# Kernel tuning notes

Measured on AMD Instinct MI355X. Metric: run time of the kernel, lower is better.

The kernel has to match this reference:

```python
import jax, jax.numpy as jnp
import numpy as np

B, L, H, DK, DV, DM = 8, 1024, 8, 80, 80, 640
LN_EPS = 1e-5


def setup_inputs() -> dict:
    key = jax.random.key(0)
    ks = jax.random.split(key, 5)
    q = jax.random.normal(ks[0], (B, L, DM), dtype=jnp.float32)
    k = jax.random.normal(ks[1], (B, L, DM), dtype=jnp.float32)
    v = jax.random.normal(ks[2], (B, L, DM), dtype=jnp.float32)
    # fc: nn.Linear(n_head*d_v, d_model), xavier-normal init
    fc_std = float(np.sqrt(2.0 / (H * DV + DM)))
    fc_w = jax.random.normal(ks[3], (DM, H * DV), dtype=jnp.float32) * fc_std
    fc_b = jnp.zeros((DM,), dtype=jnp.float32)
    gamma_1 = jnp.full((DM,), 1e-4, dtype=jnp.float32)  # init_values * ones(640)
    ln_w = jnp.ones((DM,), dtype=jnp.float32)
    ln_b = jnp.zeros((DM,), dtype=jnp.float32)
    return {"q": q, "k": k, "v": v, "fc_w": fc_w, "fc_b": fc_b,
            "gamma_1": gamma_1, "ln_w": ln_w, "ln_b": ln_b}


def reference(q, k, v, fc_w, fc_b, gamma_1, ln_w, ln_b):
    # Inputs are viewed directly into heads (projections are commented out in source).
    residual = q
    qh = q.reshape(B, L, H, DK)  # [b, q, h, d]
    kh = k.reshape(B, L, H, DK)  # [b, k, h, d]
    vh = v.reshape(B, L, H, DV)  # [b, k, h, d]

    # L2-distance attention scores: -sum((q-k)^2) = -(||q||^2 - 2 q.k + ||k||^2)
    sq = jnp.sum(qh * qh, axis=-1)                       # [b, q, h]
    sk = jnp.sum(kh * kh, axis=-1)                       # [b, k, h]
    cross = jnp.einsum('bqhd,bkhd->bhqk', qh, kh)        # [b, h, q, k]
    scores = -(sq.transpose(0, 2, 1)[:, :, :, None]
               - 2.0 * cross
               + sk.transpose(0, 2, 1)[:, :, None, :]) / 13.0

    attn = jax.nn.softmax(scores, axis=-1)               # softmax over keys (dim=2 in 3D view)
    # dropout(p=0.8) treated as identity (eval mode)

    out = jnp.einsum('bhqk,bkhd->bqhd', attn, vh)        # [b, q, h, dv]
    out = out.reshape(B, L, H * DV)
    out = out @ fc_w.T + fc_b                            # fc projection
    # dropout treated as identity (eval mode)

    x = out * gamma_1 + residual
    mu = jnp.mean(x, axis=-1, keepdims=True)
    var = jnp.mean((x - mu) ** 2, axis=-1, keepdims=True)
    y = (x - mu) * jax.lax.rsqrt(var + LN_EPS) * ln_w + ln_b
    return y
```

## Files before the change

kernel.cpp:

```cpp
#include <hip/hip_runtime.h>

#define B_ 8
#define L_ 1024
#define H_ 8
#define DM_ 640

typedef __attribute__((ext_vector_type(8))) short bf16x8;
typedef __attribute__((ext_vector_type(4))) short bf16x4;
typedef __attribute__((ext_vector_type(4))) float f32x4;
typedef __attribute__((ext_vector_type(2))) float f32x2;
typedef __attribute__((ext_vector_type(2))) int i32x2;
typedef __attribute__((ext_vector_type(4))) unsigned short us4;
typedef __attribute__((ext_vector_type(8))) unsigned short us8;

#if __has_builtin(__builtin_amdgcn_exp2f)
#define EXP2F __builtin_amdgcn_exp2f
#else
#define EXP2F exp2f
#endif

#define C1F 0.22195308f
#define C2F 0.11097654f

#define VTP_TILE_SHORTS 5184
#define ATTN8_OFF 10616832

__device__ __forceinline__ unsigned short f2bf(float f) {
  unsigned int u = __builtin_bit_cast(unsigned int, f);
  u += 0x7fffu + ((u >> 16) & 1u);
  return (unsigned short)(u >> 16);
}
__device__ __forceinline__ float bf2f(unsigned short h) {
  unsigned int u = ((unsigned int)h) << 16;
  return __builtin_bit_cast(float, u);
}
__device__ __forceinline__ float sane(float x, float lim) {
  return fminf(fmaxf(x, -lim), lim);
}
__device__ __forceinline__ unsigned cvt_pk_bf16(float a, float b) {
  unsigned r;
  asm("v_cvt_pk_bf16_f32 %0, %1, %2" : "=v"(r) : "v"(a), "v"(b));
  return r;
}

__global__ __launch_bounds__(256) void prep_kernel(
    const float* __restrict__ kg, const float* __restrict__ vg,
    unsigned short* __restrict__ Kp, unsigned short* __restrict__ Vtp) {
  __shared__ float V_lds[64 * 81];
  __shared__ float w_lds[64];
  const int tid = threadIdx.x;
  const int bh = blockIdx.x >> 4, kt = blockIdx.x & 15;
  const int b = bh >> 3, h = bh & 7;
  const int key = tid >> 2, part = tid & 3;
  const int keyg = kt * 64 + key;

  const float* krow = kg + (size_t)(b * L_ + keyg) * DM_ + h * 80 + part * 20;
  const float* vrow = vg + (size_t)(b * L_ + keyg) * DM_ + h * 80 + part * 20;
  unsigned short* kpr = Kp + ((size_t)bh * L_ + keyg) * 80 + part * 20;

  float ssq = 0.f;
#pragma unroll
  for (int i = 0; i < 5; ++i) {
    float4 f = *(const float4*)(krow + 4 * i);
    ssq += f.x * f.x + f.y * f.y + f.z * f.z + f.w * f.w;
    us4 h4 = {f2bf(f.x * C1F), f2bf(f.y * C1F), f2bf(f.z * C1F), f2bf(f.w * C1F)};
    *(us4*)(kpr + 4 * i) = h4;
    float4 g4 = *(const float4*)(vrow + 4 * i);
    int d0 = part * 20 + 4 * i;
    V_lds[key * 81 + d0 + 0] = g4.x;
    V_lds[key * 81 + d0 + 1] = g4.y;
    V_lds[key * 81 + d0 + 2] = g4.z;
    V_lds[key * 81 + d0 + 3] = g4.w;
  }
  ssq += __shfl_xor(ssq, 1);
  ssq += __shfl_xor(ssq, 2);
  if (part == 0) w_lds[key] = EXP2F((80.f - ssq) * C2F);
  __syncthreads();

  unsigned short* vt = Vtp + (size_t)(bh * 16 + kt) * VTP_TILE_SHORTS;
#pragma unroll
  for (int r = 0; r < 11; ++r) {
    int p = r * 256 + tid;
    if (p < 81 * 32) {
      int dv = p >> 5, kp = (p & 31) * 2;
      float wa = w_lds[kp], wb = w_lds[kp + 1];
      float va = (dv < 80) ? V_lds[kp * 81 + dv] * wa : wa;
      float vb = (dv < 80) ? V_lds[(kp + 1) * 81 + dv] * wb : wb;
      *(unsigned*)(vt + dv * 64 + kp) =
          (unsigned)f2bf(va) | ((unsigned)f2bf(vb) << 16);
    }
  }
}

#define KSTR 104
#define VSTR 76

__global__ __launch_bounds__(256, 2) void attn_kernel(
    const float* __restrict__ qg, const unsigned short* __restrict__ Kp,
    const unsigned short* __restrict__ Vtp, unsigned char* __restrict__ attn8) {
  __shared__ __align__(16) unsigned short K_lds[2][64 * KSTR];
  __shared__ __align__(16) unsigned short Vt_lds[2][80 * VSTR];
  __shared__ __align__(16) unsigned short w_sh[2][64];

  const int tid = threadIdx.x;
  const int wid = tid >> 6, lane = tid & 63;
  const int col = lane & 15, g = lane >> 4;
  const int bx = blockIdx.x;
  const int bh = bx & 63, qt = bx >> 6;
  const int b = bh >> 3, h = bh & 7;

  if (tid < 128) {
    us8 z = {0, 0, 0, 0, 0, 0, 0, 0};
    int bufz = tid >> 6, r = tid & 63;
    *(us8*)&K_lds[bufz][r * KSTR + 80] = z;
    *(us8*)&K_lds[bufz][r * KSTR + 88] = z;
  }

  const int ka0 = tid, ka1 = tid + 256, ka2 = tid + 512;
  const int kr0 = ka0 / 10, kc0 = ka0 - kr0 * 10;
  const int kr1 = ka1 / 10, kc1 = ka1 - kr1 * 10;
  const int kr2 = ka2 / 10, kc2 = ka2 - kr2 * 10;
  const int vr0 = ka0 >> 3, vc0 = ka0 & 7;
  const int vr1 = ka1 >> 3, vc1 = ka1 & 7;
  const int vr2 = ka2 >> 3, vc2 = ka2 & 7;

  const unsigned short* kslice = Kp + (size_t)bh * L_ * 80;
  const unsigned short* vslice = Vtp + (size_t)(bh * 16) * VTP_TILE_SHORTS;

  us8 sk0, sk1, sk2, sv0, sv1, sv2, sw;
  auto load_tile = [&](int kt) {
    const unsigned short* kb = kslice + (size_t)kt * 5120;
    const unsigned short* vb = vslice + (size_t)kt * VTP_TILE_SHORTS;
    sk0 = *(const us8*)(kb + kr0 * 80 + kc0 * 8);
    sk1 = *(const us8*)(kb + kr1 * 80 + kc1 * 8);
    if (tid < 128) sk2 = *(const us8*)(kb + kr2 * 80 + kc2 * 8);
    sv0 = *(const us8*)(vb + vr0 * 64 + vc0 * 8);
    sv1 = *(const us8*)(vb + vr1 * 64 + vc1 * 8);
    if (tid < 128) sv2 = *(const us8*)(vb + vr2 * 64 + vc2 * 8);
    if (tid < 8) sw = *(const us8*)(vb + 5120 + tid * 8);
  };
  auto write_tile = [&](int bf) {
    *(us8*)&K_lds[bf][kr0 * KSTR + kc0 * 8] = sk0;
    *(us8*)&K_lds[bf][kr1 * KSTR + kc1 * 8] = sk1;
    if (tid < 128) *(us8*)&K_lds[bf][kr2 * KSTR + kc2 * 8] = sk2;
    *(us8*)&Vt_lds[bf][vr0 * VSTR + vc0 * 8] = sv0;
    *(us8*)&Vt_lds[bf][vr1 * VSTR + vc1 * 8] = sv1;
    if (tid < 128) *(us8*)&Vt_lds[bf][vr2 * VSTR + vc2 * 8] = sv2;
    if (tid < 8) *(us8*)&w_sh[bf][tid * 8] = sw;
  };

  bf16x8 qa0[3], qa1[3];
  {
    const int qr0 = qt * 128 + wid * 16 + col;
#pragma unroll
    for (int s = 0; s < 2; ++s) {
      const float* qr = qg + (size_t)(b * L_ + qr0 + s * 64) * DM_ + h * 80;
      bf16x8* qa = s ? qa1 : qa0;
#pragma unroll
      for (int c = 0; c < 3; ++c) {
        int d0 = c * 32 + g * 8;
        if (d0 < 80) {
          float4 f0 = *(const float4*)(qr + d0);
          float4 f1 = *(const float4*)(qr + d0 + 4);
          qa[c][0] = (short)f2bf(f0.x); qa[c][1] = (short)f2bf(f0.y);
          qa[c][2] = (short)f2bf(f0.z); qa[c][3] = (short)f2bf(f0.w);
          qa[c][4] = (short)f2bf(f1.x); qa[c][5] = (short)f2bf(f1.y);
          qa[c][6] = (short)f2bf(f1.z); qa[c][7] = (short)f2bf(f1.w);
        } else {
#pragma unroll
          for (int e = 0; e < 8; ++e) qa[c][e] = 0;
        }
      }
    }
  }

  f32x4 acc_o0[5], acc_o1[5];
#pragma unroll
  for (int u = 0; u < 5; ++u) {
    f32x4 z = {0.f, 0.f, 0.f, 0.f};
    acc_o0[u] = z;
    acc_o1[u] = z;
  }
  float lp0 = 0.f, lp1 = 0.f;

  load_tile(0);
  write_tile(0);
  __syncthreads();

  for (int kt = 0; kt < 16; ++kt) {
    const int cur = kt & 1;
    if (kt < 15) load_tile(kt + 1);

    f32x4 accS0[4], accS1[4];
#pragma unroll
    for (int t = 0; t < 4; ++t) {
      f32x4 z = {0.f, 0.f, 0.f, 0.f};
      accS0[t] = z;
      accS1[t] = z;
    }
    __builtin_amdgcn_s_setprio(1);
#pragma unroll
    for (int t = 0; t < 4; ++t)
#pragma unroll
      for (int c = 0; c < 3; ++c) {
        bf16x8 kf = *(const bf16x8*)&K_lds[cur][(t * 16 + col) * KSTR + c * 32 + g * 8];
        accS0[t] = __builtin_amdgcn_mfma_f32_16x16x32_bf16(kf, qa0[c], accS0[t], 0, 0, 0);
        accS1[t] = __builtin_amdgcn_mfma_f32_16x16x32_bf16(kf, qa1[c], accS1[t], 0, 0, 0);
      }
    __builtin_amdgcn_s_setprio(0);

#pragma unroll
    for (int t = 0; t < 4; ++t) {
      us4 w4 = *(const us4*)&w_sh[cur][t * 16 + g * 4];
      float w0 = bf2f(w4[0]), w1 = bf2f(w4[1]), w2 = bf2f(w4[2]), w3 = bf2f(w4[3]);
      float p00 = EXP2F(accS0[t][0]), p01 = EXP2F(accS0[t][1]);
      float p02 = EXP2F(accS0[t][2]), p03 = EXP2F(accS0[t][3]);
      float p10 = EXP2F(accS1[t][0]), p11 = EXP2F(accS1[t][1]);
      float p12 = EXP2F(accS1[t][2]), p13 = EXP2F(accS1[t][3]);
      lp0 += p00 * w0 + p01 * w1 + p02 * w2 + p03 * w3;
      lp1 += p10 * w0 + p11 * w1 + p12 * w2 + p13 * w3;
      i32x2 pw0 = {(int)cvt_pk_bf16(p00, p01), (int)cvt_pk_bf16(p02, p03)};
      i32x2 pw1 = {(int)cvt_pk_bf16(p10, p11), (int)cvt_pk_bf16(p12, p13)};
      bf16x4 pf0 = __builtin_bit_cast(bf16x4, pw0);
      bf16x4 pf1 = __builtin_bit_cast(bf16x4, pw1);
      __builtin_amdgcn_s_setprio(1);
#pragma unroll
      for (int u = 0; u < 5; ++u) {
        bf16x4 vf = *(const bf16x4*)&Vt_lds[cur][(u * 16 + col) * VSTR + t * 16 + g * 4];
        acc_o0[u] = __builtin_amdgcn_mfma_f32_16x16x16bf16_1k(vf, pf0, acc_o0[u], 0, 0, 0);
        acc_o1[u] = __builtin_amdgcn_mfma_f32_16x16x16bf16_1k(vf, pf1, acc_o1[u], 0, 0, 0);
      }
      __builtin_amdgcn_s_setprio(0);
    }

    if (kt < 15) {
      write_tile(cur ^ 1);
      __syncthreads();
    }
  }

  float l0 = lp0 + __shfl_xor(lp0, 16);
  l0 += __shfl_xor(l0, 32);
  float l1 = lp1 + __shfl_xor(lp1, 16);
  l1 += __shfl_xor(l1, 32);
#pragma unroll
  for (int s = 0; s < 2; ++s) {
    f32x4* acc_o = s ? acc_o1 : acc_o0;
    float invl = 1.0f / fmaxf(s ? l1 : l0, 1e-30f);
    const int qrow = qt * 128 + s * 64 + wid * 16 + col;
    unsigned char* ob = attn8 + (size_t)(b * L_ + qrow) * DM_ + h * 80;
#pragma unroll
    for (int u = 0; u < 5; ++u) {
      float o0 = sane(acc_o[u][0] * invl, 240.f);
      float o1 = sane(acc_o[u][1] * invl, 240.f);
      float o2 = sane(acc_o[u][2] * invl, 240.f);
      float o3 = sane(acc_o[u][3] * invl, 240.f);
      int pk = __builtin_amdgcn_cvt_pk_fp8_f32(o0, o1, 0, false);
      pk = __builtin_amdgcn_cvt_pk_fp8_f32(o2, o3, pk, true);
      *(int*)(ob + u * 16 + g * 4) = pk;
    }
  }
}

#define BSTR 40
__global__ __launch_bounds__(256) void fc_kernel(
    const unsigned char* __restrict__ attn8, const float* __restrict__ w,
    const float* __restrict__ fcb, const float* __restrict__ gamma,
    const float* __restrict__ qres, unsigned short* __restrict__ xout) {
  __shared__ __align__(16) unsigned short A_lds[2][64 * BSTR];
  __shared__ __align__(16) unsigned short B_lds[2][64 * BSTR];

  const int tid = threadIdx.x;
  const int wid = tid >> 6, lane = tid & 63;
  const int col = lane & 15, g = lane >> 4;
  const int rt = blockIdx.x / 10, cn = blockIdx.x % 10;
  const int wm = wid >> 1, wn = wid & 1;
  const int r = tid >> 2, sg = tid & 3;

  f32x4 acc[2][2];
#pragma unroll
  for (int m = 0; m < 2; ++m)
#pragma unroll
    for (int n = 0; n < 2; ++n) {
      f32x4 z = {0.f, 0.f, 0.f, 0.f};
      acc[m][n] = z;
    }

  uint2 sa;
  float4 sb0, sb1;
  auto load_k = [&](int kc) {
    sa = *(const uint2*)(attn8 + (size_t)(rt * 64 + r) * DM_ + kc * 32 + sg * 8);
    const float* wsrc = w + (size_t)(cn * 64 + r) * DM_ + kc * 32 + sg * 8;
    sb0 = *(const float4*)wsrc;
    sb1 = *(const float4*)(wsrc + 4);
  };
  auto write_k = [&](int bf) {
    const unsigned* adw = (const unsigned*)&sa;
    unsigned ow[4];
#pragma unroll
    for (int d = 0; d < 2; ++d) {
      f32x2 lo = __builtin_amdgcn_cvt_pk_f32_fp8(adw[d], false);
      f32x2 hi = __builtin_amdgcn_cvt_pk_f32_fp8(adw[d], true);
      ow[2 * d] = cvt_pk_bf16(lo[0], lo[1]);
      ow[2 * d + 1] = cvt_pk_bf16(hi[0], hi[1]);
    }
    *(uint4*)&A_lds[bf][r * BSTR + sg * 8] =
        *(const uint4*)ow;
    unsigned bw[4] = {cvt_pk_bf16(sb0.x, sb0.y), cvt_pk_bf16(sb0.z, sb0.w),
                      cvt_pk_bf16(sb1.x, sb1.y), cvt_pk_bf16(sb1.z, sb1.w)};
    *(uint4*)&B_lds[bf][r * BSTR + sg * 8] = *(const uint4*)bw;
  };

  load_k(0);
  write_k(0);
  __syncthreads();

  for (int kc = 0; kc < 20; ++kc) {
    const int cur = kc & 1;
    if (kc < 19) load_k(kc + 1);

    bf16x8 af[2], bfr[2];
#pragma unroll
    for (int m = 0; m < 2; ++m)
      af[m] = *(const bf16x8*)&A_lds[cur][(wm * 32 + m * 16 + col) * BSTR + g * 8];
#pragma unroll
    for (int n = 0; n < 2; ++n)
      bfr[n] = *(const bf16x8*)&B_lds[cur][(wn * 32 + n * 16 + col) * BSTR + g * 8];
#pragma unroll
    for (int m = 0; m < 2; ++m)
#pragma unroll
      for (int n = 0; n < 2; ++n)
        acc[m][n] = __builtin_amdgcn_mfma_f32_16x16x32_bf16(af[m], bfr[n], acc[m][n], 0, 0, 0);

    if (kc < 19) {
      write_k(cur ^ 1);
      __syncthreads();
    }
  }

  int jcol[2];
  float fb2[2], gm[2];
#pragma unroll
  for (int n = 0; n < 2; ++n) {
    jcol[n] = cn * 64 + wn * 32 + n * 16 + col;
    fb2[n] = fcb[jcol[n]];
    gm[n] = gamma[jcol[n]];
  }
#pragma unroll
  for (int m = 0; m < 2; ++m) {
    int rowg = rt * 64 + wm * 32 + m * 16 + g * 4;
#pragma unroll
    for (int j = 0; j < 4; ++j) {
      int row = rowg + j;
#pragma unroll
      for (int n = 0; n < 2; ++n) {
        float xv = (acc[m][n][j] + fb2[n]) * gm[n] + qres[(size_t)row * DM_ + jcol[n]];
        xout[(size_t)row * DM_ + jcol[n]] = f2bf(sane(xv, 1e5f));
      }
    }
  }
}

__global__ __launch_bounds__(256) void ln_kernel(
    const unsigned short* __restrict__ x, const float* __restrict__ lw,
    const float* __restrict__ lb, float* __restrict__ y) {
  const int wid = threadIdx.x >> 6, lane = threadIdx.x & 63;
  const int row = blockIdx.x * 4 + wid;
  const unsigned short* xr = x + (size_t)row * DM_;

  unsigned int u[5];
  float s = 0.f, ss = 0.f;
#pragma unroll
  for (int i = 0; i < 5; ++i) {
    u[i] = *(const unsigned int*)(xr + 2 * (lane + 64 * i));
    float a0 = bf2f((unsigned short)(u[i] & 0xffff));
    float a1 = bf2f((unsigned short)(u[i] >> 16));
    s += a0 + a1;
    ss += a0 * a0 + a1 * a1;
  }
#pragma unroll
  for (int d = 1; d < 64; d <<= 1) {
    s += __shfl_xor(s, d);
    ss += __shfl_xor(ss, d);
  }
  const float mu = s * (1.f / 640.f);
  const float var = ss * (1.f / 640.f) - mu * mu;
  const float rstd = rsqrtf(var + 1e-5f);

  float* yr = y + (size_t)row * DM_;
#pragma unroll
  for (int i = 0; i < 5; ++i) {
    int c0 = 2 * (lane + 64 * i);
    float a0 = bf2f((unsigned short)(u[i] & 0xffff));
    float a1 = bf2f((unsigned short)(u[i] >> 16));
    float2 wv = *(const float2*)(lw + c0);
    float2 bv = *(const float2*)(lb + c0);
    float2 out;
    out.x = (a0 - mu) * rstd * wv.x + bv.x;
    out.y = (a1 - mu) * rstd * wv.y + bv.y;
    *(float2*)(yr + c0) = out;
  }
}

extern "C" void kernel_launch(void* const* d_in, const int* in_sizes, int n_in,
                              void* d_out, int out_size, void* d_ws, size_t ws_size,
                              hipStream_t stream) {
  const float* q = (const float*)d_in[0];
  const float* k = (const float*)d_in[1];
  const float* v = (const float*)d_in[2];
  const float* fw = (const float*)d_in[3];
  const float* fb = (const float*)d_in[4];
  const float* g1 = (const float*)d_in[5];
  const float* lw = (const float*)d_in[6];
  const float* lb = (const float*)d_in[7];

  unsigned short* vtp = (unsigned short*)d_out;
  unsigned char* attn8 = (unsigned char*)d_out + ATTN8_OFF;
  unsigned short* kp = (unsigned short*)d_ws;
  unsigned short* xws = (unsigned short*)d_ws;
  float* y = (float*)d_out;

  prep_kernel<<<dim3(64 * 16), dim3(256), 0, stream>>>(k, v, kp, vtp);
  attn_kernel<<<dim3(64 * 8), dim3(256), 0, stream>>>(q, kp, vtp, attn8);
  fc_kernel<<<dim3(128 * 10), dim3(256), 0, stream>>>(attn8, fw, fb, g1, q, xws);
  ln_kernel<<<dim3(8192 / 4), dim3(256), 0, stream>>>(xws, lw, lb, y);
}
```

Measured before the change: 84.01 us.

## Switch QK score path to FP8 MFMA and halve queries per attention block

K is now prepped as FP8 in padded 96-byte rows and Q is converted to FP8, so the score GEMM uses the 16x16x32 fp8 MFMA instead of bf16. This halves K global and LDS traffic. Each attention block now handles 64 queries instead of 128, doubling the grid to 1024 blocks and raising launch bounds to 4 waves per SIMD for more occupancy. In exchange, scores lose precision because FP8 enters inside the exponent, and K tiles are reused across fewer queries per block.

```diff
diff --git a/kernel.cpp b/kernel.cpp
--- a/kernel.cpp
+++ b/kernel.cpp
@@ -24,6 +24,7 @@
 
 #define VTP_TILE_SHORTS 5184
 #define ATTN8_OFF 10616832
+#define KP_ROW_B 96
 
 __device__ __forceinline__ unsigned short f2bf(float f) {
   unsigned int u = __builtin_bit_cast(unsigned int, f);
@@ -45,7 +46,7 @@
 
 __global__ __launch_bounds__(256) void prep_kernel(
     const float* __restrict__ kg, const float* __restrict__ vg,
-    unsigned short* __restrict__ Kp, unsigned short* __restrict__ Vtp) {
+    unsigned char* __restrict__ Kp8, unsigned short* __restrict__ Vtp) {
   __shared__ float V_lds[64 * 81];
   __shared__ float w_lds[64];
   const int tid = threadIdx.x;
@@ -56,21 +57,26 @@
 
   const float* krow = kg + (size_t)(b * L_ + keyg) * DM_ + h * 80 + part * 20;
   const float* vrow = vg + (size_t)(b * L_ + keyg) * DM_ + h * 80 + part * 20;
-  unsigned short* kpr = Kp + ((size_t)bh * L_ + keyg) * 80 + part * 20;
+  unsigned char* kpr = Kp8 + ((size_t)bh * L_ + keyg) * KP_ROW_B + part * 20;
 
   float ssq = 0.f;
 #pragma unroll
   for (int i = 0; i < 5; ++i) {
     float4 f = *(const float4*)(krow + 4 * i);
     ssq += f.x * f.x + f.y * f.y + f.z * f.z + f.w * f.w;
-    us4 h4 = {f2bf(f.x * C1F), f2bf(f.y * C1F), f2bf(f.z * C1F), f2bf(f.w * C1F)};
-    *(us4*)(kpr + 4 * i) = h4;
+    int pk = __builtin_amdgcn_cvt_pk_fp8_f32(f.x * C1F, f.y * C1F, 0, false);
+    pk = __builtin_amdgcn_cvt_pk_fp8_f32(f.z * C1F, f.w * C1F, pk, true);
+    *(unsigned*)(kpr + 4 * i) = (unsigned)pk;
     float4 g4 = *(const float4*)(vrow + 4 * i);
     int d0 = part * 20 + 4 * i;
     V_lds[key * 81 + d0 + 0] = g4.x;
     V_lds[key * 81 + d0 + 1] = g4.y;
     V_lds[key * 81 + d0 + 2] = g4.z;
     V_lds[key * 81 + d0 + 3] = g4.w;
+  }
+  if (part == 0) {
+    uint4 z = {0, 0, 0, 0};
+    *(uint4*)(Kp8 + ((size_t)bh * L_ + keyg) * KP_ROW_B + 80) = z;
   }
   ssq += __shfl_xor(ssq, 1);
   ssq += __shfl_xor(ssq, 2);
@@ -92,13 +98,13 @@
   }
 }
 
-#define KSTR 104
+#define KSTRB 112
 #define VSTR 76
 
-__global__ __launch_bounds__(256, 2) void attn_kernel(
-    const float* __restrict__ qg, const unsigned short* __restrict__ Kp,
+__global__ __launch_bounds__(256, 4) void attn_kernel(
+    const float* __restrict__ qg, const unsigned char* __restrict__ Kp8,
     const unsigned short* __restrict__ Vtp, unsigned char* __restrict__ attn8) {
-  __shared__ __align__(16) unsigned short K_lds[2][64 * KSTR];
+  __shared__ __align__(16) unsigned char K_lds[2][64 * KSTRB];
   __shared__ __align__(16) unsigned short Vt_lds[2][80 * VSTR];
   __shared__ __align__(16) unsigned short w_sh[2][64];
 
@@ -109,79 +115,67 @@
   const int bh = bx & 63, qt = bx >> 6;
   const int b = bh >> 3, h = bh & 7;
 
-  if (tid < 128) {
-    us8 z = {0, 0, 0, 0, 0, 0, 0, 0};
-    int bufz = tid >> 6, r = tid & 63;
-    *(us8*)&K_lds[bufz][r * KSTR + 80] = z;
-    *(us8*)&K_lds[bufz][r * KSTR + 88] = z;
-  }
-
-  const int ka0 = tid, ka1 = tid + 256, ka2 = tid + 512;
-  const int kr0 = ka0 / 10, kc0 = ka0 - kr0 * 10;
-  const int kr1 = ka1 / 10, kc1 = ka1 - kr1 * 10;
-  const int kr2 = ka2 / 10, kc2 = ka2 - kr2 * 10;
-  const int vr0 = ka0 >> 3, vc0 = ka0 & 7;
-  const int vr1 = ka1 >> 3, vc1 = ka1 & 7;
-  const int vr2 = ka2 >> 3, vc2 = ka2 & 7;
-
-  const unsigned short* kslice = Kp + (size_t)bh * L_ * 80;
+  const int kf0 = tid, kf1 = tid + 256;
+  const int kr0 = kf0 / 6, kc0 = kf0 - kr0 * 6;
+  const int kr1 = kf1 / 6, kc1 = kf1 - kr1 * 6;
+  const int va0 = tid, va1 = tid + 256, va2 = tid + 512;
+  const int vr0 = va0 >> 3, vc0 = va0 & 7;
+  const int vr1 = va1 >> 3, vc1 = va1 & 7;
+  const int vr2 = va2 >> 3, vc2 = va2 & 7;
+
+  const unsigned char* kslice = Kp8 + (size_t)bh * L_ * KP_ROW_B;
   const unsigned short* vslice = Vtp + (size_t)(bh * 16) * VTP_TILE_SHORTS;
 
-  us8 sk0, sk1, sk2, sv0, sv1, sv2, sw;
+  uint4 sk0, sk1;
+  us8 sv0, sv1, sv2, sw;
   auto load_tile = [&](int kt) {
-    const unsigned short* kb = kslice + (size_t)kt * 5120;
+    const unsigned char* kb = kslice + (size_t)kt * 64 * KP_ROW_B;
     const unsigned short* vb = vslice + (size_t)kt * VTP_TILE_SHORTS;
-    sk0 = *(const us8*)(kb + kr0 * 80 + kc0 * 8);
-    sk1 = *(const us8*)(kb + kr1 * 80 + kc1 * 8);
-    if (tid < 128) sk2 = *(const us8*)(kb + kr2 * 80 + kc2 * 8);
+    sk0 = *(const uint4*)(kb + kr0 * KP_ROW_B + kc0 * 16);
+    if (tid < 128) sk1 = *(const uint4*)(kb + kr1 * KP_ROW_B + kc1 * 16);
     sv0 = *(const us8*)(vb + vr0 * 64 + vc0 * 8);
     sv1 = *(const us8*)(vb + vr1 * 64 + vc1 * 8);
     if (tid < 128) sv2 = *(const us8*)(vb + vr2 * 64 + vc2 * 8);
     if (tid < 8) sw = *(const us8*)(vb + 5120 + tid * 8);
   };
   auto write_tile = [&](int bf) {
-    *(us8*)&K_lds[bf][kr0 * KSTR + kc0 * 8] = sk0;
-    *(us8*)&K_lds[bf][kr1 * KSTR + kc1 * 8] = sk1;
-    if (tid < 128) *(us8*)&K_lds[bf][kr2 * KSTR + kc2 * 8] = sk2;
+    *(uint4*)&K_lds[bf][kr0 * KSTRB + kc0 * 16] = sk0;
+    if (tid < 128) *(uint4*)&K_lds[bf][kr1 * KSTRB + kc1 * 16] = sk1;
     *(us8*)&Vt_lds[bf][vr0 * VSTR + vc0 * 8] = sv0;
     *(us8*)&Vt_lds[bf][vr1 * VSTR + vc1 * 8] = sv1;
     if (tid < 128) *(us8*)&Vt_lds[bf][vr2 * VSTR + vc2 * 8] = sv2;
     if (tid < 8) *(us8*)&w_sh[bf][tid * 8] = sw;
   };
 
-  bf16x8 qa0[3], qa1[3];
+  long qa[3];
   {
-    const int qr0 = qt * 128 + wid * 16 + col;
-#pragma unroll
-    for (int s = 0; s < 2; ++s) {
-      const float* qr = qg + (size_t)(b * L_ + qr0 + s * 64) * DM_ + h * 80;
-      bf16x8* qa = s ? qa1 : qa0;
-#pragma unroll
-      for (int c = 0; c < 3; ++c) {
-        int d0 = c * 32 + g * 8;
-        if (d0 < 80) {
-          float4 f0 = *(const float4*)(qr + d0);
-          float4 f1 = *(const float4*)(qr + d0 + 4);
-          qa[c][0] = (short)f2bf(f0.x); qa[c][1] = (short)f2bf(f0.y);
-          qa[c][2] = (short)f2bf(f0.z); qa[c][3] = (short)f2bf(f0.w);
-          qa[c][4] = (short)f2bf(f1.x); qa[c][5] = (short)f2bf(f1.y);
-          qa[c][6] = (short)f2bf(f1.z); qa[c][7] = (short)f2bf(f1.w);
-        } else {
-#pragma unroll
-          for (int e = 0; e < 8; ++e) qa[c][e] = 0;
-        }
+    const int qrow = qt * 64 + wid * 16 + col;
+    const float* qr = qg + (size_t)(b * L_ + qrow) * DM_ + h * 80;
+#pragma unroll
+    for (int c = 0; c < 3; ++c) {
+      int d0 = c * 32 + g * 8;
+      if (d0 < 80) {
+        float4 f0 = *(const float4*)(qr + d0);
+        float4 f1 = *(const float4*)(qr + d0 + 4);
+        int lo = __builtin_amdgcn_cvt_pk_fp8_f32(f0.x, f0.y, 0, false);
+        lo = __builtin_amdgcn_cvt_pk_fp8_f32(f0.z, f0.w, lo, true);
+        int hi = __builtin_amdgcn_cvt_pk_fp8_f32(f1.x, f1.y, 0, false);
+        hi = __builtin_amdgcn_cvt_pk_fp8_f32(f1.z, f1.w, hi, true);
+        i32x2 q2 = {lo, hi};
+        qa[c] = __builtin_bit_cast(long, q2);
+      } else {
+        qa[c] = 0;
       }
     }
   }
 
-  f32x4 acc_o0[5], acc_o1[5];
+  f32x4 acc_o[5];
 #pragma unroll
   for (int u = 0; u < 5; ++u) {
     f32x4 z = {0.f, 0.f, 0.f, 0.f};
-    acc_o0[u] = z;
-    acc_o1[u] = z;
-  }
-  float lp0 = 0.f, lp1 = 0.f;
+    acc_o[u] = z;
+  }
+  float lp = 0.f;
 
   load_tile(0);
   write_tile(0);
@@ -191,46 +185,37 @@
     const int cur = kt & 1;
     if (kt < 15) load_tile(kt + 1);
 
-    f32x4 accS0[4], accS1[4];
+    f32x4 accS[4];
 #pragma unroll
     for (int t = 0; t < 4; ++t) {
       f32x4 z = {0.f, 0.f, 0.f, 0.f};
-      accS0[t] = z;
-      accS1[t] = z;
-    }
-    __builtin_amdgcn_s_setprio(1);
-#pragma unroll
-    for (int t = 0; t < 4; ++t)
-#pragma unroll
-      for (int c = 0; c < 3; ++c) {
-        bf16x8 kf = *(const bf16x8*)&K_lds[cur][(t * 16 + col) * KSTR + c * 32 + g * 8];
-        accS0[t] = __builtin_amdgcn_mfma_f32_16x16x32_bf16(kf, qa0[c], accS0[t], 0, 0, 0);
-        accS1[t] = __builtin_amdgcn_mfma_f32_16x16x32_bf16(kf, qa1[c], accS1[t], 0, 0, 0);
-      }
-    __builtin_amdgcn_s_setprio(0);
+      accS[t] = z;
+    }
+#pragma unroll
+    for (int t = 0; t < 4; ++t) {
+      const unsigned char* tb = &K_lds[cur][(t * 16 + col) * KSTRB];
+      long k0 = *(const long*)(tb + g * 8);
+      long k1 = *(const long*)(tb + 32 + g * 8);
+      long k2 = *(const long*)(tb + 64 + g * 8);
+      accS[t] = __builtin_amdgcn_mfma_f32_16x16x32_fp8_fp8(k0, qa[0], accS[t], 0, 0, 0);
+      accS[t] = __builtin_amdgcn_mfma_f32_16x16x32_fp8_fp8(k1, qa[1], accS[t], 0, 0, 0);
+      accS[t] = __builtin_amdgcn_mfma_f32_16x16x32_fp8_fp8(k2, qa[2], accS[t], 0, 0, 0);
+    }
 
 #pragma unroll
     for (int t = 0; t < 4; ++t) {
       us4 w4 = *(const us4*)&w_sh[cur][t * 16 + g * 4];
       float w0 = bf2f(w4[0]), w1 = bf2f(w4[1]), w2 = bf2f(w4[2]), w3 = bf2f(w4[3]);
-      float p00 = EXP2F(accS0[t][0]), p01 = EXP2F(accS0[t][1]);
-      float p02 = EXP2F(accS0[t][2]), p03 = EXP2F(accS0[t][3]);
-      float p10 = EXP2F(accS1[t][0]), p11 = EXP2F(accS1[t][1]);
-      float p12 = EXP2F(accS1[t][2]), p13 = EXP2F(accS1[t][3]);
-      lp0 += p00 * w0 + p01 * w1 + p02 * w2 + p03 * w3;
-      lp1 += p10 * w0 + p11 * w1 + p12 * w2 + p13 * w3;
-      i32x2 pw0 = {(int)cvt_pk_bf16(p00, p01), (int)cvt_pk_bf16(p02, p03)};
-      i32x2 pw1 = {(int)cvt_pk_bf16(p10, p11), (int)cvt_pk_bf16(p12, p13)};
-      bf16x4 pf0 = __builtin_bit_cast(bf16x4, pw0);
-      bf16x4 pf1 = __builtin_bit_cast(bf16x4, pw1);
-      __builtin_amdgcn_s_setprio(1);
+      float p0 = EXP2F(accS[t][0]), p1 = EXP2F(accS[t][1]);
+      float p2 = EXP2F(accS[t][2]), p3 = EXP2F(accS[t][3]);
+      lp += p0 * w0 + p1 * w1 + p2 * w2 + p3 * w3;
+      i32x2 pw = {(int)cvt_pk_bf16(p0, p1), (int)cvt_pk_bf16(p2, p3)};
+      bf16x4 pf = __builtin_bit_cast(bf16x4, pw);
 #pragma unroll
       for (int u = 0; u < 5; ++u) {
         bf16x4 vf = *(const bf16x4*)&Vt_lds[cur][(u * 16 + col) * VSTR + t * 16 + g * 4];
-        acc_o0[u] = __builtin_amdgcn_mfma_f32_16x16x16bf16_1k(vf, pf0, acc_o0[u], 0, 0, 0);
-        acc_o1[u] = __builtin_amdgcn_mfma_f32_16x16x16bf16_1k(vf, pf1, acc_o1[u], 0, 0, 0);
+        acc_o[u] = __builtin_amdgcn_mfma_f32_16x16x16bf16_1k(vf, pf, acc_o[u], 0, 0, 0);
       }
-      __builtin_amdgcn_s_setprio(0);
     }
 
     if (kt < 15) {
@@ -239,26 +224,20 @@
     }
   }
 
-  float l0 = lp0 + __shfl_xor(lp0, 16);
-  l0 += __shfl_xor(l0, 32);
-  float l1 = lp1 + __shfl_xor(lp1, 16);
-  l1 += __shfl_xor(l1, 32);
-#pragma unroll
-  for (int s = 0; s < 2; ++s) {
-    f32x4* acc_o = s ? acc_o1 : acc_o0;
-    float invl = 1.0f / fmaxf(s ? l1 : l0, 1e-30f);
-    const int qrow = qt * 128 + s * 64 + wid * 16 + col;
-    unsigned char* ob = attn8 + (size_t)(b * L_ + qrow) * DM_ + h * 80;
-#pragma unroll
-    for (int u = 0; u < 5; ++u) {
-      float o0 = sane(acc_o[u][0] * invl, 240.f);
-      float o1 = sane(acc_o[u][1] * invl, 240.f);
-      float o2 = sane(acc_o[u][2] * invl, 240.f);
-      float o3 = sane(acc_o[u][3] * invl, 240.f);
-      int pk = __builtin_amdgcn_cvt_pk_fp8_f32(o0, o1, 0, false);
-      pk = __builtin_amdgcn_cvt_pk_fp8_f32(o2, o3, pk, true);
-      *(int*)(ob + u * 16 + g * 4) = pk;
-    }
+  float l = lp + __shfl_xor(lp, 16);
+  l += __shfl_xor(l, 32);
+  float invl = 1.0f / fmaxf(l, 1e-30f);
+  const int qrow = qt * 64 + wid * 16 + col;
+  unsigned char* ob = attn8 + (size_t)(b * L_ + qrow) * DM_ + h * 80;
+#pragma unroll
+  for (int u = 0; u < 5; ++u) {
+    float o0 = sane(acc_o[u][0] * invl, 240.f);
+    float o1 = sane(acc_o[u][1] * invl, 240.f);
+    float o2 = sane(acc_o[u][2] * invl, 240.f);
+    float o3 = sane(acc_o[u][3] * invl, 240.f);
+    int pk = __builtin_amdgcn_cvt_pk_fp8_f32(o0, o1, 0, false);
+    pk = __builtin_amdgcn_cvt_pk_fp8_f32(o2, o3, pk, true);
+    *(int*)(ob + u * 16 + g * 4) = pk;
   }
 }
 
@@ -304,8 +283,7 @@
       ow[2 * d] = cvt_pk_bf16(lo[0], lo[1]);
       ow[2 * d + 1] = cvt_pk_bf16(hi[0], hi[1]);
     }
-    *(uint4*)&A_lds[bf][r * BSTR + sg * 8] =
-        *(const uint4*)ow;
+    *(uint4*)&A_lds[bf][r * BSTR + sg * 8] = *(const uint4*)ow;
     unsigned bw[4] = {cvt_pk_bf16(sb0.x, sb0.y), cvt_pk_bf16(sb0.z, sb0.w),
                       cvt_pk_bf16(sb1.x, sb1.y), cvt_pk_bf16(sb1.z, sb1.w)};
     *(uint4*)&B_lds[bf][r * BSTR + sg * 8] = *(const uint4*)bw;
@@ -416,12 +394,12 @@
 
   unsigned short* vtp = (unsigned short*)d_out;
   unsigned char* attn8 = (unsigned char*)d_out + ATTN8_OFF;
-  unsigned short* kp = (unsigned short*)d_ws;
+  unsigned char* kp8 = (unsigned char*)d_ws;
   unsigned short* xws = (unsigned short*)d_ws;
   float* y = (float*)d_out;
 
-  prep_kernel<<<dim3(64 * 16), dim3(256), 0, stream>>>(k, v, kp, vtp);
-  attn_kernel<<<dim3(64 * 8), dim3(256), 0, stream>>>(q, kp, vtp, attn8);
+  prep_kernel<<<dim3(64 * 16), dim3(256), 0, stream>>>(k, v, kp8, vtp);
+  attn_kernel<<<dim3(64 * 16), dim3(256), 0, stream>>>(q, kp8, vtp, attn8);
   fc_kernel<<<dim3(128 * 10), dim3(256), 0, stream>>>(attn8, fw, fb, g1, q, xws);
   ln_kernel<<<dim3(8192 / 4), dim3(256), 0, stream>>>(xws, lw, lb, y);
 }
```

Result: no change. 84.75 us (+0.9%).
